# Optimization experiments

Measured on AMD Instinct MI355X. Metric: run time of the kernel, lower is better.

## Reference

```python
import jax, jax.numpy as jnp
import numpy as np

B, S, D = 4, 2048, 1024
H = 4 * D          # expert hidden dim
E_SPEC = 4         # num specific experts
E_SHR = 2          # num shared experts
TOP_K = 2


def setup_inputs() -> dict:
    key = jax.random.key(0)
    ks = jax.random.split(key, 16)
    s = 0.02
    return {
        "x": jax.random.normal(ks[0], (B, S, D), jnp.float32),
        # specific experts (stacked over expert axis)
        "spec_w1": jax.random.normal(ks[1], (E_SPEC, D, H), jnp.float32) * s,
        "spec_b1": jnp.zeros((E_SPEC, H), jnp.float32),
        "spec_w2": jax.random.normal(ks[2], (E_SPEC, H, D), jnp.float32) * s,
        "spec_b2": jnp.zeros((E_SPEC, D), jnp.float32),
        "spec_rw": jax.random.normal(ks[3], (D, E_SPEC), jnp.float32) * s,
        "spec_rb": jnp.zeros((E_SPEC,), jnp.float32),
        # shared experts
        "shr_w1": jax.random.normal(ks[4], (E_SHR, D, H), jnp.float32) * s,
        "shr_b1": jnp.zeros((E_SHR, H), jnp.float32),
        "shr_w2": jax.random.normal(ks[5], (E_SHR, H, D), jnp.float32) * s,
        "shr_b2": jnp.zeros((E_SHR, D), jnp.float32),
        "shr_rw": jax.random.normal(ks[6], (D, E_SHR), jnp.float32) * s,
        "shr_rb": jnp.zeros((E_SHR,), jnp.float32),
    }


def _expert_mlp(xf, w1, b1, w2, b2):
    # xf: [T, D]; w1: [E, D, H]; w2: [E, H, D] -> [E, T, D]
    h = jax.nn.gelu(jnp.einsum("td,edh->eth", xf, w1) + b1[:, None, :],
                    approximate=False)
    return jnp.einsum("eth,ehd->etd", h, w2) + b2[:, None, :]


def reference(x, spec_w1, spec_b1, spec_w2, spec_b2, spec_rw, spec_rb,
              shr_w1, shr_b1, shr_w2, shr_b2, shr_rw, shr_rb):
    b, s, d = x.shape
    xf = x.reshape(-1, d)                      # [T, D]
    T = xf.shape[0]

    # --- specific (top-k) routing ---
    spec_probs = jax.nn.softmax(xf @ spec_rw + spec_rb, axis=-1)   # [T, E]
    topk_probs, topk_idx = jax.lax.top_k(spec_probs, TOP_K)        # [T, K]

    # aux load-balancing loss
    counts = jnp.zeros((E_SPEC,), jnp.float32).at[topk_idx.reshape(-1)].add(1.0)
    fraction = counts / (T * TOP_K)
    aux_loss = E_SPEC * jnp.sum(fraction * spec_probs.mean(axis=0))

    # gate[t, e] = sum_k topk_probs[t,k] * 1[topk_idx[t,k]==e]
    gate = jnp.sum(jax.nn.one_hot(topk_idx, E_SPEC, dtype=xf.dtype)
                   * topk_probs[..., None], axis=1)                # [T, E]

    spec_out_e = _expert_mlp(xf, spec_w1, spec_b1, spec_w2, spec_b2)  # [E, T, D]
    specific_out = jnp.einsum("te,etd->td", gate, spec_out_e)

    # --- shared (dense) experts ---
    shr_probs = jax.nn.softmax(xf @ shr_rw + shr_rb, axis=-1)      # [T, E_shr]
    shr_out_e = _expert_mlp(xf, shr_w1, shr_b1, shr_w2, shr_b2)    # [E_shr, T, D]
    shared_out = jnp.einsum("te,etd->td", shr_probs, shr_out_e)

    final = (specific_out + shared_out).reshape(b, s, d)
    return final, aux_loss
```

## Files before the change

kernel.cpp:

```cpp
#include <hip/hip_runtime.h>
#include <hip/hip_bf16.h>

#define T_TOK 8192
#define DDIM 1024
#define HDIM 4096

typedef __bf16 bf16;
typedef bf16 bf16x8 __attribute__((ext_vector_type(8)));
typedef float f32x4 __attribute__((ext_vector_type(4)));

#define ASM_VMCNT(n) asm volatile("s_waitcnt vmcnt(" #n ")" ::: "memory")
#define MFMA16(a, b, c) __builtin_amdgcn_mfma_f32_16x16x32_bf16((a), (b), (c), 0, 0, 0)
#define G8_BAR __builtin_amdgcn_s_barrier()
#define G8_WAIT                                            \
  asm volatile("s_waitcnt lgkmcnt(0)" ::: "memory");       \
  __builtin_amdgcn_sched_barrier(0)

__device__ __forceinline__ void gl_lds16(const void* g, void* l) {
  __builtin_amdgcn_global_load_lds(
      (const __attribute__((address_space(1))) unsigned int*)g,
      (__attribute__((address_space(3))) unsigned int*)l, 16, 0, 0);
}

__device__ __forceinline__ float gelu_f(float v) {
  const float x = v * 0.7071067811865475f;
  const float ax = fabsf(x);
  const float t = 1.0f / fmaf(0.3275911f, ax, 1.0f);
  float p = fmaf(1.061405429f, t, -1.453152027f);
  p = fmaf(p, t, 1.421413741f);
  p = fmaf(p, t, -0.284496736f);
  p = fmaf(p, t, 0.254829592f);
  p = p * t;
  const float e = __expf(-ax * ax);
  const float er = fmaf(-p, e, 1.0f);
  const float erfx = (x >= 0.0f) ? er : -er;
  return 0.5f * v * (1.0f + erfx);
}

__global__ __launch_bounds__(256) void conv_router(
    const float* __restrict__ x, bf16* __restrict__ xb,
    const float* __restrict__ srw, const float* __restrict__ srb,
    const float* __restrict__ hrw, const float* __restrict__ hrb,
    float* __restrict__ gate, float4* __restrict__ probs4,
    int* __restrict__ top2) {
  const int lane = threadIdx.x & 63;
  const int w = threadIdx.x >> 6;
  const int t = blockIdx.x * 4 + w;

  const float* xr = x + (size_t)t * DDIM;
  bf16* xbr = xb + (size_t)t * DDIM;
  float p0 = 0, p1 = 0, p2 = 0, p3 = 0, p4 = 0, p5 = 0;
#pragma unroll
  for (int c = 0; c < 4; ++c) {
    const int d = c * 256 + lane * 4;
    const float4 xv = *(const float4*)(xr + d);
    bf16 ov[4] = {(bf16)xv.x, (bf16)xv.y, (bf16)xv.z, (bf16)xv.w};
    *(float2*)(xbr + d) = *(float2*)ov;
    const float xa[4] = {xv.x, xv.y, xv.z, xv.w};
#pragma unroll
    for (int j = 0; j < 4; ++j) {
      const float xd = xa[j];
      const float4 r4 = *(const float4*)(srw + (size_t)(d + j) * 4);
      p0 += xd * r4.x; p1 += xd * r4.y; p2 += xd * r4.z; p3 += xd * r4.w;
      const float2 r2 = *(const float2*)(hrw + (size_t)(d + j) * 2);
      p4 += xd * r2.x; p5 += xd * r2.y;
    }
  }
#pragma unroll
  for (int off = 32; off >= 1; off >>= 1) {
    p0 += __shfl_xor(p0, off);
    p1 += __shfl_xor(p1, off);
    p2 += __shfl_xor(p2, off);
    p3 += __shfl_xor(p3, off);
    p4 += __shfl_xor(p4, off);
    p5 += __shfl_xor(p5, off);
  }
  if (lane == 0) {
    const float l0 = p0 + srb[0], l1 = p1 + srb[1];
    const float l2 = p2 + srb[2], l3 = p3 + srb[3];
    const float m = fmaxf(fmaxf(l0, l1), fmaxf(l2, l3));
    const float e0 = expf(l0 - m), e1 = expf(l1 - m);
    const float e2 = expf(l2 - m), e3 = expf(l3 - m);
    const float s = e0 + e1 + e2 + e3;
    float pr[4] = {e0 / s, e1 / s, e2 / s, e3 / s};
    int i1 = 0; float v1 = pr[0];
#pragma unroll
    for (int e = 1; e < 4; ++e) if (pr[e] > v1) { v1 = pr[e]; i1 = e; }
    int i2 = -1; float v2 = -1.0f;
#pragma unroll
    for (int e = 0; e < 4; ++e)
      if (e != i1 && pr[e] > v2) { v2 = pr[e]; i2 = e; }
    float g[4] = {0, 0, 0, 0};
    g[i1] = v1; g[i2] = v2;
    float* gr = gate + (size_t)t * 8;
    gr[0] = g[0]; gr[1] = g[1]; gr[2] = g[2]; gr[3] = g[3];
    const float h0 = p4 + hrb[0], h1 = p5 + hrb[1];
    const float mh = fmaxf(h0, h1);
    const float q0 = expf(h0 - mh), q1 = expf(h1 - mh);
    const float qs = q0 + q1;
    gr[4] = q0 / qs; gr[5] = q1 / qs; gr[6] = 0; gr[7] = 0;
    probs4[t] = make_float4(pr[0], pr[1], pr[2], pr[3]);
    top2[t] = i1 | (i2 << 8);
  }
}

__global__ __launch_bounds__(256) void transpose_convert6(
    const float* __restrict__ spec_w, const float* __restrict__ shr_w,
    bf16* __restrict__ dst, int R, int C) {
  __shared__ float tile[32][33];
  const int z = blockIdx.z;
  const float* src = (z < 4) ? spec_w + (size_t)z * R * C
                             : shr_w + (size_t)(z - 4) * R * C;
  bf16* d = dst + (size_t)z * R * C;
  const int c0 = blockIdx.x * 32, r0 = blockIdx.y * 32;
  const int tx = threadIdx.x & 31, ty = threadIdx.x >> 5;
#pragma unroll
  for (int i = 0; i < 4; ++i)
    tile[ty + 8 * i][tx] = src[(size_t)(r0 + ty + 8 * i) * C + c0 + tx];
  __syncthreads();
#pragma unroll
  for (int i = 0; i < 4; ++i)
    d[(size_t)(c0 + ty + 8 * i) * R + r0 + tx] = (bf16)tile[tx][ty + 8 * i];
}

__global__ __launch_bounds__(1024) void scan_build(
    const int* __restrict__ top2, const float4* __restrict__ probs4,
    int* __restrict__ meta, int* __restrict__ lists, int2* __restrict__ tpos,
    float* __restrict__ auxg) {
  __shared__ unsigned long long sc[1024];
  __shared__ float4 rp[512];
  const int tid = threadIdx.x;

  int ee[8];
  unsigned long long c = 0;
  float4 ps = make_float4(0.f, 0.f, 0.f, 0.f);
#pragma unroll
  for (int j = 0; j < 8; ++j) {
    const int t = tid * 8 + j;
    const int p = top2[t];
    ee[j] = p;
    const int a = p & 15, b = (p >> 8) & 15;
    c += (1ULL << (16 * a)) + (1ULL << (16 * b));
    const float4 pv = probs4[t];
    ps.x += pv.x; ps.y += pv.y; ps.z += pv.z; ps.w += pv.w;
  }
  sc[tid] = c;
  __syncthreads();
  for (int off = 1; off < 1024; off <<= 1) {
    const unsigned long long mine = sc[tid];
    const unsigned long long prev = (tid >= off) ? sc[tid - off] : 0ULL;
    __syncthreads();
    sc[tid] = mine + prev;
    __syncthreads();
  }
  const unsigned long long incl = sc[tid];
  const unsigned long long tot = sc[1023];
  const unsigned long long excl = incl - c;
  int q0 = (int)(excl & 0xffff), q1 = (int)((excl >> 16) & 0xffff);
  int q2 = (int)((excl >> 32) & 0xffff), q3 = (int)((excl >> 48) & 0xffff);
#pragma unroll
  for (int j = 0; j < 8; ++j) {
    const int t = tid * 8 + j;
    const int a = ee[j] & 15, b = (ee[j] >> 8) & 15;
    const int pa = (a == 0) ? q0 : (a == 1) ? q1 : (a == 2) ? q2 : q3;
    lists[a * 8192 + pa] = t;
    q0 += (a == 0); q1 += (a == 1); q2 += (a == 2); q3 += (a == 3);
    const int pb = (b == 0) ? q0 : (b == 1) ? q1 : (b == 2) ? q2 : q3;
    lists[b * 8192 + pb] = t;
    q0 += (b == 0); q1 += (b == 1); q2 += (b == 2); q3 += (b == 3);
    tpos[t] = make_int2(a * 8192 + pa, b * 8192 + pb);
  }
  if (tid == 1023) {
    const int c0 = (int)(tot & 0xffff), c1 = (int)((tot >> 16) & 0xffff);
    const int c2 = (int)((tot >> 32) & 0xffff), c3 = (int)((tot >> 48) & 0xffff);
    meta[24] = c0; meta[25] = c1; meta[26] = c2; meta[27] = c3;
    auxg[0] = (float)c0; auxg[1] = (float)c1;
    auxg[2] = (float)c2; auxg[3] = (float)c3;
    const int nb0 = (c0 + 255) >> 8, nb1 = (c1 + 255) >> 8;
    const int nb2 = (c2 + 255) >> 8, nb3 = (c3 + 255) >> 8;
    const int ch0 = (nb0 + 3) >> 2, ch1 = (nb1 + 3) >> 2;
    const int ch2 = (nb2 + 3) >> 2, ch3 = (nb3 + 3) >> 2;
    meta[34] = 0;
    meta[35] = nb0 * 256;
    meta[36] = meta[35] + nb1 * 256;
    meta[37] = meta[36] + nb2 * 256;
    meta[40] = 0;
    meta[41] = 64 * ch0;
    meta[42] = meta[41] + 64 * ch1;
    meta[43] = meta[42] + 64 * ch2;
    meta[44] = meta[43] + 64 * ch3;
    meta[46] = 0;
    meta[47] = 32 * ch0;
    meta[48] = meta[47] + 32 * ch1;
    meta[49] = meta[48] + 32 * ch2;
    meta[50] = meta[49] + 32 * ch3;
  }
  if (tid >= 512) rp[tid - 512] = ps;
  __syncthreads();
  if (tid < 512) {
    const float4 o = rp[tid];
    ps.x += o.x; ps.y += o.y; ps.z += o.z; ps.w += o.w;
  }
  for (int w = 256; w >= 1; w >>= 1) {
    __syncthreads();
    if (tid >= w && tid < 2 * w) rp[tid - w] = ps;
    __syncthreads();
    if (tid < w) {
      const float4 o = rp[tid];
      ps.x += o.x; ps.y += o.y; ps.z += o.z; ps.w += o.w;
    }
  }
  if (tid == 0) {
    auxg[4] = ps.x; auxg[5] = ps.y; auxg[6] = ps.z; auxg[7] = ps.w;
  }
}

__global__ void aux_finalize(const float* __restrict__ auxg,
                             float* __restrict__ outp) {
  float a = 0.0f;
#pragma unroll
  for (int e = 0; e < 4; ++e)
    a += (auxg[e] / (float)(T_TOK * 2)) * (auxg[4 + e] / (float)T_TOK);
  outp[0] = 4.0f * a;
}

template <int KIND>
__global__ __launch_bounds__(512, 2) void g8(
    const bf16* __restrict__ A, const bf16* __restrict__ Bw,
    const float* __restrict__ bias, bf16* __restrict__ h_all, int N,
    int CH_M, int CH_N, const int* __restrict__ meta,
    const int* __restrict__ lists) {
  __shared__ __align__(1024) bf16 Alds[2 * 256 * 64];
  __shared__ __align__(1024) bf16 Blds[2 * 256 * 64];

  const int tid = threadIdx.x;
  const int lane = tid & 63, wid = tid >> 6;
  const int wm = wid >> 2, wn = wid & 3;
  const int lr = lane & 15, lg = lane >> 4;

  int bm, bn, hb = 0, s = 0;
  const bf16* Bp = Bw;
  const float* biasp = bias;
  if constexpr (KIND == 0) {
    const int xcd = blockIdx.x & 7, idx = blockIdx.x >> 3;
    bm = (xcd >> 1) * CH_M + idx / CH_N;
    bn = (xcd & 1) * CH_N + idx % CH_N;
  } else {
    const int b = blockIdx.x;
    if (b >= meta[44]) return;
    s = (b >= meta[41]) + (b >= meta[42]) + (b >= meta[43]);
    const int local = b - meta[40 + s];
    const int nbm = (meta[24 + s] + 255) >> 8;
    const int CHm = (nbm + 3) >> 2;
    if (local >= 64 * CHm) return;
    const int xc = local & 7, idx = local >> 3;
    bm = (xc >> 1) * CHm + idx / 8;
    bn = (xc & 1) * 8 + idx % 8;
    if (bm >= nbm) return;
    hb = meta[34 + s];
    Bp = Bw + (size_t)s * DDIM * HDIM;
    biasp = bias + (size_t)s * HDIM;
  }
  const int K = DDIM;
  const int NT = K >> 6;

  const int rl = tid >> 3;
  const int cbs = ((tid * 16) & 127) ^ ((rl & 7) << 4);
  int ar[4];
#pragma unroll
  for (int c = 0; c < 4; ++c) ar[c] = bm * 256 + c * 64 + rl;
  if constexpr (KIND != 0) {
    const int* lp = lists + s * 8192;
#pragma unroll
    for (int c = 0; c < 4; ++c) {
      const int t = lp[ar[c]];
      ar[c] = t < 0 ? 0 : t;
    }
  }
  const bf16* sA[4];
  const bf16* sB[4];
#pragma unroll
  for (int c = 0; c < 4; ++c) {
    sA[c] = A + (size_t)ar[c] * K + (cbs >> 1);
    sB[c] = Bp + (size_t)(bn * 256 + c * 64 + rl) * K + (cbs >> 1);
  }
  char* const ldsA = (char*)Alds;
  char* const ldsB = (char*)Blds;
  const int wb = wid * 1024;

  const int ax0 = (lg * 16) ^ ((lr & 7) << 4);
  const int ax1 = ax0 ^ 64;
  const int aro = (wm * 128 + lr) * 128;
  const int bro = (wn * 64 + lr) * 128;
  const char* const A0 = (const char*)Alds + aro + ax0;
  const char* const A1 = (const char*)Alds + aro + ax1;
  const char* const B0 = (const char*)Blds + bro + ax0;
  const char* const B1 = (const char*)Blds + bro + ax1;

  f32x4 acc[8][4] = {};
  bf16x8 af[4][2], b01[2][2], b23[2][2];

#define G8_RA(BOFF, MB)                                               \
  _Pragma("unroll") for (int i = 0; i < 4; ++i) {                     \
    af[i][0] = *(const bf16x8*)(A0 + (BOFF) + ((MB) + i) * 2048);     \
    af[i][1] = *(const bf16x8*)(A1 + (BOFF) + ((MB) + i) * 2048);     \
  }
#define G8_RB(BOFF, DST, NB)                                          \
  _Pragma("unroll") for (int i = 0; i < 2; ++i) {                     \
    DST[i][0] = *(const bf16x8*)(B0 + (BOFF) + ((NB) + i) * 2048);    \
    DST[i][1] = *(const bf16x8*)(B1 + (BOFF) + ((NB) + i) * 2048);    \
  }
#define G8_MMA(MB, NB, BSRC)                                          \
  __builtin_amdgcn_s_setprio(1);                                      \
  _Pragma("unroll") for (int i = 0; i < 4; ++i)                       \
    _Pragma("unroll") for (int j = 0; j < 2; ++j) {                   \
      acc[(MB) + i][(NB) + j] =                                       \
          MFMA16(af[i][0], BSRC[j][0], acc[(MB) + i][(NB) + j]);      \
      acc[(MB) + i][(NB) + j] =                                       \
          MFMA16(af[i][1], BSRC[j][1], acc[(MB) + i][(NB) + j]);      \
    }                                                                 \
  __builtin_amdgcn_s_setprio(0);
#define G8_STG_B(T, C, BUFO)                                          \
  gl_lds16(sB[C] + (size_t)(T) * 64, ldsB + (BUFO) + (C) * 8192 + wb);
#define G8_STG_A(T, C, BUFO)                                          \
  gl_lds16(sA[C] + (size_t)(T) * 64, ldsA + (BUFO) + (C) * 8192 + wb);

  G8_STG_B(0, 0, 0) G8_STG_B(0, 1, 0) G8_STG_B(0, 2, 0) G8_STG_B(0, 3, 0)
  G8_STG_A(0, 0, 0) G8_STG_A(0, 1, 0) G8_STG_A(0, 2, 0) G8_STG_A(0, 3, 0)
  G8_STG_B(1, 0, 32768) G8_STG_B(1, 1, 32768)
  G8_STG_B(1, 2, 32768) G8_STG_B(1, 3, 32768)
  G8_STG_A(1, 0, 32768) G8_STG_A(1, 1, 32768)
  G8_STG_A(1, 2, 32768) G8_STG_A(1, 3, 32768)
  ASM_VMCNT(8);
  G8_BAR;

  for (int t = 0; t < NT; t += 2) {
    const bool stg = (t + 2) < NT;
    G8_RA(0, 0);
    G8_RB(0, b01, 0);
    G8_BAR; G8_WAIT;
    G8_MMA(0, 0, b01);
    G8_BAR;
    G8_RB(0, b23, 2);
    G8_BAR; G8_WAIT;
    G8_MMA(0, 2, b23);
    G8_BAR;
    G8_RA(0, 4);
    if (stg) { G8_STG_B(t + 2, 0, 0) G8_STG_B(t + 2, 1, 0) }
    G8_BAR; G8_WAIT;
    G8_MMA(4, 0, b01);
    G8_BAR;
    if (stg) { G8_STG_B(t + 2, 2, 0) G8_STG_B(t + 2, 3, 0) }
    G8_MMA(4, 2, b23);
    if (stg) ASM_VMCNT(4); else ASM_VMCNT(0);
    G8_BAR;
    G8_RA(32768, 0);
    G8_RB(32768, b01, 0);
    if (stg) { G8_STG_A(t + 2, 0, 0) G8_STG_A(t + 2, 1, 0) }
    G8_BAR; G8_WAIT;
    G8_MMA(0, 0, b01);
    G8_BAR;
    G8_RB(32768, b23, 2);
    if (stg) { G8_STG_A(t + 2, 2, 0) G8_STG_A(t + 2, 3, 0) }
    G8_BAR; G8_WAIT;
    G8_MMA(0, 2, b23);
    G8_BAR;
    G8_RA(32768, 4);
    if (stg) {
      G8_STG_B(t + 3, 0, 32768) G8_STG_B(t + 3, 1, 32768)
      G8_STG_B(t + 3, 2, 32768) G8_STG_B(t + 3, 3, 32768)
    }
    G8_BAR; G8_WAIT;
    G8_MMA(4, 0, b01);
    G8_BAR;
    if (stg) {
      G8_STG_A(t + 3, 0, 32768) G8_STG_A(t + 3, 1, 32768)
      G8_STG_A(t + 3, 2, 32768) G8_STG_A(t + 3, 3, 32768)
    }
    G8_MMA(4, 2, b23);
    if (stg) ASM_VMCNT(8);
    G8_BAR;
  }

  const int colb = bn * 256 + wn * 64;
  const int rowb = hb + bm * 256 + wm * 128 + lg * 4;
  float bv[4];
#pragma unroll
  for (int nf = 0; nf < 4; ++nf) bv[nf] = biasp[colb + nf * 16 + lr];
#pragma unroll
  for (int mf = 0; mf < 8; ++mf)
#pragma unroll
    for (int nf = 0; nf < 4; ++nf) {
      const int col = colb + nf * 16 + lr;
#pragma unroll
      for (int r = 0; r < 4; ++r) {
        const int row = rowb + mf * 16 + r;
        h_all[(size_t)row * N + col] = (bf16)gelu_f(acc[mf][nf][r] + bv[nf]);
      }
    }
}

template <int EMODE>
__global__ __launch_bounds__(512, 2) void g2k(
    const bf16* __restrict__ A, int lda, const bf16* __restrict__ B,
    const float* __restrict__ bias, float* __restrict__ out,
    const float* __restrict__ gate, int gidx) {
  __shared__ __align__(1024) bf16 Alds[2 * 256 * 64];
  __shared__ __align__(1024) bf16 Blds[2 * 128 * 64];

  const int tid = threadIdx.x;
  const int lane = tid & 63, wid = tid >> 6;
  const int wm = wid >> 2, wn = wid & 3;
  const int lr = lane & 15, lg = lane >> 4;

  const int xcd = blockIdx.x & 7, idx = blockIdx.x >> 3;
  const int bm = (xcd >> 1) * 8 + idx / 4;
  const int bn = (xcd & 1) * 4 + idx % 4;
  const int K = HDIM, N = DDIM;
  const int NT = K >> 6;

  const int L = tid * 16;
  const int rl = L >> 7;
  const int colb = (L & 127) ^ ((rl & 7) << 4);

  const int ar0 = bm * 256 + rl;
  const bf16* sAc0 = A + (size_t)ar0 * lda + (colb >> 1);
  const bf16* sAc1 = A + (size_t)(ar0 + 64) * lda + (colb >> 1);
  const bf16* sAc2 = A + (size_t)(ar0 + 128) * lda + (colb >> 1);
  const bf16* sAc3 = A + (size_t)(ar0 + 192) * lda + (colb >> 1);
  const bf16* sB = B + (size_t)(bn * 128 + rl) * K + (colb >> 1);

  char* const ldsA = (char*)Alds;
  char* const ldsB = (char*)Blds;
  const int wb = wid * 1024;
  char* const stA[2] = {ldsA + wb, ldsA + 32768 + wb};
  char* const stB[2] = {ldsB + wb, ldsB + 16384 + wb};

  const int ax0 = (lg * 16) ^ ((lr & 7) << 4);
  const int ax1 = ax0 ^ 64;
  const int aro = (wm * 128 + lr) * 128;
  const int bro = (wn * 32 + lr) * 128;
  const char* const Ak0[2] = {ldsA + aro + ax0, ldsA + 32768 + aro + ax0};
  const char* const Ak1[2] = {ldsA + aro + ax1, ldsA + 32768 + aro + ax1};
  const char* const Bk0[2] = {ldsB + bro + ax0, ldsB + 16384 + bro + ax0};
  const char* const Bk1[2] = {ldsB + bro + ax1, ldsB + 16384 + bro + ax1};

  f32x4 acc[8][2] = {};

  gl_lds16(sAc0, stA[0]);
  gl_lds16(sAc1, stA[0] + 8192);
  gl_lds16(sAc2, stA[0] + 16384);
  gl_lds16(sAc3, stA[0] + 24576);
  gl_lds16(sB, stB[0]);
  gl_lds16(sB + (size_t)64 * K, stB[0] + 8192);
  gl_lds16(sB + 64, stB[1]);
  gl_lds16(sB + (size_t)64 * K + 64, stB[1] + 8192);
  gl_lds16(sAc0 + 64, stA[1]);
  gl_lds16(sAc1 + 64, stA[1] + 8192);
  ASM_VMCNT(4);
  __builtin_amdgcn_s_barrier();

  for (int kt0 = 0; kt0 < NT; kt0 += 2) {
#pragma unroll
    for (int par = 0; par < 2; ++par) {
      const int kt = kt0 + par;
      const int cur = par, oth = par ^ 1;
      const bool st1 = (kt + 1) < NT, st2 = (kt + 2) < NT;
      const size_t ko1 = (size_t)(kt + 1) << 6, ko2 = (size_t)(kt + 2) << 6;
      const char* Ac0 = Ak0[cur]; const char* Ac1 = Ak1[cur];
      const char* Bc0 = Bk0[cur]; const char* Bc1 = Bk1[cur];

      bf16x8 af[4][2], bfr[2][2];

#pragma unroll
      for (int mf = 0; mf < 4; ++mf) {
        af[mf][0] = *(const bf16x8*)(Ac0 + mf * 2048);
        af[mf][1] = *(const bf16x8*)(Ac1 + mf * 2048);
      }
      bfr[0][0] = *(const bf16x8*)(Bc0);
      bfr[0][1] = *(const bf16x8*)(Bc1);
      if (st1) {
        gl_lds16(sAc2 + ko1, stA[oth] + 16384);
        gl_lds16(sAc3 + ko1, stA[oth] + 24576);
      }
      __builtin_amdgcn_s_barrier();
      asm volatile("s_waitcnt lgkmcnt(0)" ::: "memory");
      __builtin_amdgcn_sched_barrier(0);
      __builtin_amdgcn_s_setprio(1);
#pragma unroll
      for (int mf = 0; mf < 4; ++mf) {
        acc[mf][0] = MFMA16(af[mf][0], bfr[0][0], acc[mf][0]);
        acc[mf][0] = MFMA16(af[mf][1], bfr[0][1], acc[mf][0]);
      }
      __builtin_amdgcn_s_setprio(0);
      __builtin_amdgcn_s_barrier();

      bfr[1][0] = *(const bf16x8*)(Bc0 + 2048);
      bfr[1][1] = *(const bf16x8*)(Bc1 + 2048);
      __builtin_amdgcn_s_barrier();
      asm volatile("s_waitcnt lgkmcnt(0)" ::: "memory");
      __builtin_amdgcn_sched_barrier(0);
      __builtin_amdgcn_s_setprio(1);
#pragma unroll
      for (int mf = 0; mf < 4; ++mf) {
        acc[mf][1] = MFMA16(af[mf][0], bfr[1][0], acc[mf][1]);
        acc[mf][1] = MFMA16(af[mf][1], bfr[1][1], acc[mf][1]);
      }
      __builtin_amdgcn_s_setprio(0);
      __builtin_amdgcn_s_barrier();

#pragma unroll
      for (int mf = 0; mf < 4; ++mf) {
        af[mf][0] = *(const bf16x8*)(Ac0 + 8192 + mf * 2048);
        af[mf][1] = *(const bf16x8*)(Ac1 + 8192 + mf * 2048);
      }
      if (st2) {
        gl_lds16(sB + ko2, stB[cur]);
        gl_lds16(sB + (size_t)64 * K + ko2, stB[cur] + 8192);
      }
      __builtin_amdgcn_s_barrier();
      asm volatile("s_waitcnt lgkmcnt(0)" ::: "memory");
      __builtin_amdgcn_sched_barrier(0);
      __builtin_amdgcn_s_setprio(1);
#pragma unroll
      for (int mf = 0; mf < 4; ++mf) {
        acc[4 + mf][0] = MFMA16(af[mf][0], bfr[0][0], acc[4 + mf][0]);
        acc[4 + mf][0] = MFMA16(af[mf][1], bfr[0][1], acc[4 + mf][0]);
      }
      __builtin_amdgcn_s_setprio(0);
      __builtin_amdgcn_s_barrier();

      if (st2) {
        gl_lds16(sAc0 + ko2, stA[cur]);
        gl_lds16(sAc1 + ko2, stA[cur] + 8192);
      }
      __builtin_amdgcn_s_setprio(1);
#pragma unroll
      for (int mf = 0; mf < 4; ++mf) {
        acc[4 + mf][1] = MFMA16(af[mf][0], bfr[1][0], acc[4 + mf][1]);
        acc[4 + mf][1] = MFMA16(af[mf][1], bfr[1][1], acc[4 + mf][1]);
      }
      __builtin_amdgcn_s_setprio(0);
      if (st2) {
        ASM_VMCNT(4);
        __builtin_amdgcn_s_barrier();
      } else if (st1) {
        ASM_VMCNT(0);
        __builtin_amdgcn_s_barrier();
      }
    }
  }

  const int colb2 = bn * 128 + wn * 32;
  const int rowb = bm * 256 + wm * 128 + lg * 4;
  float bv[2];
#pragma unroll
  for (int nf = 0; nf < 2; ++nf) bv[nf] = bias[colb2 + nf * 16 + lr];
#pragma unroll
  for (int mf = 0; mf < 8; ++mf) {
    float gv[4];
#pragma unroll
    for (int r = 0; r < 4; ++r)
      gv[r] = gate[(size_t)(rowb + mf * 16 + r) * 8 + gidx];
#pragma unroll
    for (int nf = 0; nf < 2; ++nf) {
      const int col = colb2 + nf * 16 + lr;
#pragma unroll
      for (int r = 0; r < 4; ++r) {
        const float v = acc[mf][nf][r] + bv[nf];
        const size_t oi = (size_t)(rowb + mf * 16 + r) * N + col;
        if constexpr (EMODE == 1)
          out[oi] += gv[r] * v;
        else
          out[oi] = gv[r] * v;
      }
    }
  }
}

__global__ __launch_bounds__(512, 2) void g2sp(
    const bf16* __restrict__ h_all, const bf16* __restrict__ w2t,
    const float* __restrict__ spec_b2, bf16* __restrict__ P,
    const float* __restrict__ gate, const int* __restrict__ meta,
    const int* __restrict__ lists) {
  __shared__ __align__(1024) bf16 Alds[2 * 256 * 64];
  __shared__ __align__(1024) bf16 Blds[2 * 128 * 64];

  const int tid = threadIdx.x;
  const int lane = tid & 63, wid = tid >> 6;
  const int wm = wid >> 2, wn = wid & 3;
  const int lr = lane & 15, lg = lane >> 4;

  const int b = blockIdx.x;
  if (b >= meta[50]) return;
  const int s = (b >= meta[47]) + (b >= meta[48]) + (b >= meta[49]);
  const int local = b - meta[46 + s];
  const int nbm = (meta[24 + s] + 255) >> 8;
  const int CHm = (nbm + 3) >> 2;
  if (local >= 32 * CHm) return;
  const int xc = local & 7, idx = local >> 3;
  int bm = (xc >> 1) * CHm + idx / 4;
  int bn = (xc & 1) * 4 + idx % 4;
  if (bm >= nbm) return;

  const int hb = meta[34 + s];
  const bf16* B = w2t + (size_t)s * DDIM * HDIM;
  const float* bias = spec_b2 + (size_t)s * DDIM;
  const int K = HDIM, N = DDIM;
  const int NT = K >> 6;

  const int L = tid * 16;
  const int rl = L >> 7;
  const int colb = (L & 127) ^ ((rl & 7) << 4);

  const int ar0 = hb + bm * 256 + rl;
  const bf16* sAc0 = h_all + (size_t)ar0 * K + (colb >> 1);
  const bf16* sAc1 = h_all + (size_t)(ar0 + 64) * K + (colb >> 1);
  const bf16* sAc2 = h_all + (size_t)(ar0 + 128) * K + (colb >> 1);
  const bf16* sAc3 = h_all + (size_t)(ar0 + 192) * K + (colb >> 1);
  const bf16* sB = B + (size_t)(bn * 128 + rl) * K + (colb >> 1);

  char* const ldsA = (char*)Alds;
  char* const ldsB = (char*)Blds;
  const int wb = wid * 1024;
  char* const stA[2] = {ldsA + wb, ldsA + 32768 + wb};
  char* const stB[2] = {ldsB + wb, ldsB + 16384 + wb};

  const int ax0 = (lg * 16) ^ ((lr & 7) << 4);
  const int ax1 = ax0 ^ 64;
  const int aro = (wm * 128 + lr) * 128;
  const int bro = (wn * 32 + lr) * 128;
  const char* const Ak0[2] = {ldsA + aro + ax0, ldsA + 32768 + aro + ax0};
  const char* const Ak1[2] = {ldsA + aro + ax1, ldsA + 32768 + aro + ax1};
  const char* const Bk0[2] = {ldsB + bro + ax0, ldsB + 16384 + bro + ax0};
  const char* const Bk1[2] = {ldsB + bro + ax1, ldsB + 16384 + bro + ax1};

  f32x4 acc[8][2] = {};

  gl_lds16(sAc0, stA[0]);
  gl_lds16(sAc1, stA[0] + 8192);
  gl_lds16(sAc2, stA[0] + 16384);
  gl_lds16(sAc3, stA[0] + 24576);
  gl_lds16(sB, stB[0]);
  gl_lds16(sB + (size_t)64 * K, stB[0] + 8192);
  gl_lds16(sB + 64, stB[1]);
  gl_lds16(sB + (size_t)64 * K + 64, stB[1] + 8192);
  gl_lds16(sAc0 + 64, stA[1]);
  gl_lds16(sAc1 + 64, stA[1] + 8192);
  ASM_VMCNT(4);
  __builtin_amdgcn_s_barrier();

  for (int kt0 = 0; kt0 < NT; kt0 += 2) {
#pragma unroll
    for (int par = 0; par < 2; ++par) {
      const int kt = kt0 + par;
      const int cur = par, oth = par ^ 1;
      const bool st1 = (kt + 1) < NT, st2 = (kt + 2) < NT;
      const size_t ko1 = (size_t)(kt + 1) << 6, ko2 = (size_t)(kt + 2) << 6;
      const char* Ac0 = Ak0[cur]; const char* Ac1 = Ak1[cur];
      const char* Bc0 = Bk0[cur]; const char* Bc1 = Bk1[cur];

      bf16x8 af[4][2], bfr[2][2];

#pragma unroll
      for (int mf = 0; mf < 4; ++mf) {
        af[mf][0] = *(const bf16x8*)(Ac0 + mf * 2048);
        af[mf][1] = *(const bf16x8*)(Ac1 + mf * 2048);
      }
      bfr[0][0] = *(const bf16x8*)(Bc0);
      bfr[0][1] = *(const bf16x8*)(Bc1);
      if (st1) {
        gl_lds16(sAc2 + ko1, stA[oth] + 16384);
        gl_lds16(sAc3 + ko1, stA[oth] + 24576);
      }
      __builtin_amdgcn_s_barrier();
      asm volatile("s_waitcnt lgkmcnt(0)" ::: "memory");
      __builtin_amdgcn_sched_barrier(0);
      __builtin_amdgcn_s_setprio(1);
#pragma unroll
      for (int mf = 0; mf < 4; ++mf) {
        acc[mf][0] = MFMA16(af[mf][0], bfr[0][0], acc[mf][0]);
        acc[mf][0] = MFMA16(af[mf][1], bfr[0][1], acc[mf][0]);
      }
      __builtin_amdgcn_s_setprio(0);
      __builtin_amdgcn_s_barrier();

      bfr[1][0] = *(const bf16x8*)(Bc0 + 2048);
      bfr[1][1] = *(const bf16x8*)(Bc1 + 2048);
      __builtin_amdgcn_s_barrier();
      asm volatile("s_waitcnt lgkmcnt(0)" ::: "memory");
      __builtin_amdgcn_sched_barrier(0);
      __builtin_amdgcn_s_setprio(1);
#pragma unroll
      for (int mf = 0; mf < 4; ++mf) {
        acc[mf][1] = MFMA16(af[mf][0], bfr[1][0], acc[mf][1]);
        acc[mf][1] = MFMA16(af[mf][1], bfr[1][1], acc[mf][1]);
      }
      __builtin_amdgcn_s_setprio(0);
      __builtin_amdgcn_s_barrier();

#pragma unroll
      for (int mf = 0; mf < 4; ++mf) {
        af[mf][0] = *(const bf16x8*)(Ac0 + 8192 + mf * 2048);
        af[mf][1] = *(const bf16x8*)(Ac1 + 8192 + mf * 2048);
      }
      if (st2) {
        gl_lds16(sB + ko2, stB[cur]);
        gl_lds16(sB + (size_t)64 * K + ko2, stB[cur] + 8192);
      }
      __builtin_amdgcn_s_barrier();
      asm volatile("s_waitcnt lgkmcnt(0)" ::: "memory");
      __builtin_amdgcn_sched_barrier(0);
      __builtin_amdgcn_s_setprio(1);
#pragma unroll
      for (int mf = 0; mf < 4; ++mf) {
        acc[4 + mf][0] = MFMA16(af[mf][0], bfr[0][0], acc[4 + mf][0]);
        acc[4 + mf][0] = MFMA16(af[mf][1], bfr[0][1], acc[4 + mf][0]);
      }
      __builtin_amdgcn_s_setprio(0);
      __builtin_amdgcn_s_barrier();

      if (st2) {
        gl_lds16(sAc0 + ko2, stA[cur]);
        gl_lds16(sAc1 + ko2, stA[cur] + 8192);
      }
      __builtin_amdgcn_s_setprio(1);
#pragma unroll
      for (int mf = 0; mf < 4; ++mf) {
        acc[4 + mf][1] = MFMA16(af[mf][0], bfr[1][0], acc[4 + mf][1]);
        acc[4 + mf][1] = MFMA16(af[mf][1], bfr[1][1], acc[4 + mf][1]);
      }
      __builtin_amdgcn_s_setprio(0);
      if (st2) {
        ASM_VMCNT(4);
        __builtin_amdgcn_s_barrier();
      } else if (st1) {
        ASM_VMCNT(0);
        __builtin_amdgcn_s_barrier();
      }
    }
  }

  const int colb2 = bn * 128 + wn * 32;
  const int rowb = bm * 256 + wm * 128 + lg * 4;
  float bv[2];
#pragma unroll
  for (int nf = 0; nf < 2; ++nf) bv[nf] = bias[colb2 + nf * 16 + lr];
  const int* lp = lists + s * 8192;
#pragma unroll
  for (int mf = 0; mf < 8; ++mf) {
    int tok[4]; float gv[4];
#pragma unroll
    for (int r = 0; r < 4; ++r) {
      tok[r] = lp[rowb + mf * 16 + r];
      gv[r] = tok[r] >= 0 ? gate[(size_t)tok[r] * 8 + s] : 0.0f;
    }
#pragma unroll
    for (int nf = 0; nf < 2; ++nf) {
      const int col = colb2 + nf * 16 + lr;
#pragma unroll
      for (int r = 0; r < 4; ++r) {
        const float v = gv[r] * (acc[mf][nf][r] + bv[nf]);
        P[(size_t)(hb + rowb + mf * 16 + r) * N + col] = (bf16)v;
      }
    }
  }
}

__global__ __launch_bounds__(256) void reduce_spec(
    const bf16* __restrict__ P, const int2* __restrict__ tpos,
    const int* __restrict__ meta, float* __restrict__ out) {
  const int t = blockIdx.x;
  const int c = threadIdx.x * 4;
  const int2 tp = tpos[t];
  const int ea = tp.x >> 13, pa = tp.x & 8191;
  const int eb = tp.y >> 13, pb = tp.y & 8191;
  const bf16* A4 = &P[(size_t)(meta[34 + ea] + pa) * DDIM + c];
  const bf16* B4 = &P[(size_t)(meta[34 + eb] + pb) * DDIM + c];
  float4 o = *(float4*)&out[(size_t)t * DDIM + c];
  o.x += (float)A4[0] + (float)B4[0];
  o.y += (float)A4[1] + (float)B4[1];
  o.z += (float)A4[2] + (float)B4[2];
  o.w += (float)A4[3] + (float)B4[3];
  *(float4*)&out[(size_t)t * DDIM + c] = o;
}

extern "C" void kernel_launch(void* const* d_in, const int* in_sizes, int n_in,
                              void* d_out, int out_size, void* d_ws,
                              size_t ws_size, hipStream_t stream) {
  const float* x = (const float*)d_in[0];
  const float* spec_w1 = (const float*)d_in[1];
  const float* spec_b1 = (const float*)d_in[2];
  const float* spec_w2 = (const float*)d_in[3];
  const float* spec_b2 = (const float*)d_in[4];
  const float* spec_rw = (const float*)d_in[5];
  const float* spec_rb = (const float*)d_in[6];
  const float* shr_w1 = (const float*)d_in[7];
  const float* shr_b1 = (const float*)d_in[8];
  const float* shr_w2 = (const float*)d_in[9];
  const float* shr_b2 = (const float*)d_in[10];
  const float* shr_rw = (const float*)d_in[11];
  const float* shr_rb = (const float*)d_in[12];
  float* out = (float*)d_out;

  char* ws = (char*)d_ws;
  const size_t DH = (size_t)DDIM * HDIM;
  const size_t OFF_W1 = 16777216;
  const size_t OFF_W2 = OFF_W1 + 50331648;
  const size_t OFF_GATE = OFF_W2 + 50331648;
  const size_t OFF_AUX = OFF_GATE + 262144;
  const size_t OFF_META = OFF_AUX + 256;
  const size_t OFF_LIST = OFF_META + 256;
  const size_t OFF_T2 = OFF_LIST + 131072;
  const size_t OFF_P4 = OFF_T2 + 32768;
  const size_t OFF_TPOS = OFF_P4 + 131072 + 1024;
  const size_t OFF_H = OFF_TPOS + 65536;
  bf16* xb = (bf16*)ws;
  bf16* w1t = (bf16*)(ws + OFF_W1);
  bf16* w2t = (bf16*)(ws + OFF_W2);
  float* gate = (float*)(ws + OFF_GATE);
  float* auxg = (float*)(ws + OFF_AUX);
  int* meta = (int*)(ws + OFF_META);
  int* lists = (int*)(ws + OFF_LIST);
  int* top2 = (int*)(ws + OFF_T2);
  float4* probs4 = (float4*)(ws + OFF_P4);
  int2* tpos = (int2*)(ws + OFF_TPOS);
  bf16* h = (bf16*)(ws + OFF_H);
  bf16* P = w1t;

  hipMemsetAsync(lists, 0xFF, 4 * 8192 * 4, stream);

  conv_router<<<T_TOK / 4, 256, 0, stream>>>(x, xb, spec_rw, spec_rb, shr_rw,
                                             shr_rb, gate, probs4, top2);
  scan_build<<<1, 1024, 0, stream>>>(top2, probs4, meta, lists, tpos, auxg);

  transpose_convert6<<<dim3(HDIM / 32, DDIM / 32, 6), 256, 0, stream>>>(
      spec_w1, shr_w1, w1t, DDIM, HDIM);
  transpose_convert6<<<dim3(DDIM / 32, HDIM / 32, 6), 256, 0, stream>>>(
      spec_w2, shr_w2, w2t, HDIM, DDIM);

  g8<0><<<1024, 512, 0, stream>>>(xb, w1t + 4 * DH, shr_b1, h, 8192,
                                  8, 16, meta, lists);
  g2k<0><<<256, 512, 0, stream>>>(h, 8192, w2t + 4 * DH, shr_b2, out,
                                  gate, 4);
  g2k<1><<<256, 512, 0, stream>>>(h + 4096, 8192, w2t + 5 * DH,
                                  shr_b2 + 1024, out, gate, 5);
  g8<1><<<2048, 512, 0, stream>>>(xb, w1t, spec_b1, h, 4096,
                                  0, 8, meta, lists);
  g2sp<<<1024, 512, 0, stream>>>(h, w2t, spec_b2, P, gate, meta, lists);
  reduce_spec<<<T_TOK, 256, 0, stream>>>(P, tpos, meta, out);

  aux_finalize<<<1, 1, 0, stream>>>(auxg, out + (size_t)T_TOK * DDIM);
}
```

Baseline: 888.7 us.

## Swap tile shapes between first and second expert GEMMs

The first-layer GEMMs (shared and routed) now use a 256x128 tile kernel with a 2-stage pipeline, launching more blocks. The routed second-layer GEMM now uses the larger 256x256 tile kernel (K=4096) with gated output written in its epilogue. Block-offset metadata is recomputed for the new grid sizes. The aim is better wave balance on the short-K first layer and more reuse on the long-K second layer, at the cost of different LDS and register pressure per kernel.

```diff
diff --git a/kernel.cpp b/kernel.cpp
--- a/kernel.cpp
+++ b/kernel.cpp
@@ -185,15 +185,15 @@
     meta[36] = meta[35] + nb1 * 256;
     meta[37] = meta[36] + nb2 * 256;
     meta[40] = 0;
-    meta[41] = 64 * ch0;
-    meta[42] = meta[41] + 64 * ch1;
-    meta[43] = meta[42] + 64 * ch2;
-    meta[44] = meta[43] + 64 * ch3;
-    meta[46] = 0;
-    meta[47] = 32 * ch0;
-    meta[48] = meta[47] + 32 * ch1;
-    meta[49] = meta[48] + 32 * ch2;
-    meta[50] = meta[49] + 32 * ch3;
+    meta[41] = 128 * ch0;
+    meta[42] = meta[41] + 128 * ch1;
+    meta[43] = meta[42] + 128 * ch2;
+    meta[44] = meta[43] + 128 * ch3;
+    meta[52] = 0;
+    meta[53] = 16 * ch0;
+    meta[54] = meta[53] + 16 * ch1;
+    meta[55] = meta[54] + 16 * ch2;
+    meta[56] = meta[55] + 16 * ch3;
   }
   if (tid >= 512) rp[tid - 512] = ps;
   __syncthreads();
@@ -225,13 +225,12 @@
 }
 
 template <int KIND>
-__global__ __launch_bounds__(512, 2) void g8(
+__global__ __launch_bounds__(512, 2) void g1p(
     const bf16* __restrict__ A, const bf16* __restrict__ Bw,
     const float* __restrict__ bias, bf16* __restrict__ h_all, int N,
-    int CH_M, int CH_N, const int* __restrict__ meta,
-    const int* __restrict__ lists) {
+    const int* __restrict__ meta, const int* __restrict__ lists) {
   __shared__ __align__(1024) bf16 Alds[2 * 256 * 64];
-  __shared__ __align__(1024) bf16 Blds[2 * 256 * 64];
+  __shared__ __align__(1024) bf16 Blds[2 * 128 * 64];
 
   const int tid = threadIdx.x;
   const int lane = tid & 63, wid = tid >> 6;
@@ -243,8 +242,8 @@
   const float* biasp = bias;
   if constexpr (KIND == 0) {
     const int xcd = blockIdx.x & 7, idx = blockIdx.x >> 3;
-    bm = (xcd >> 1) * CH_M + idx / CH_N;
-    bn = (xcd & 1) * CH_N + idx % CH_N;
+    bm = (xcd >> 1) * 8 + idx / 32;
+    bn = (xcd & 1) * 32 + idx % 32;
   } else {
     const int b = blockIdx.x;
     if (b >= meta[44]) return;
@@ -252,31 +251,214 @@
     const int local = b - meta[40 + s];
     const int nbm = (meta[24 + s] + 255) >> 8;
     const int CHm = (nbm + 3) >> 2;
-    if (local >= 64 * CHm) return;
+    if (local >= 128 * CHm) return;
     const int xc = local & 7, idx = local >> 3;
-    bm = (xc >> 1) * CHm + idx / 8;
-    bn = (xc & 1) * 8 + idx % 8;
+    bm = (xc >> 1) * CHm + idx / 16;
+    bn = (xc & 1) * 16 + idx % 16;
     if (bm >= nbm) return;
     hb = meta[34 + s];
     Bp = Bw + (size_t)s * DDIM * HDIM;
     biasp = bias + (size_t)s * HDIM;
   }
   const int K = DDIM;
-  const int NT = K >> 6;
+  const int NT = 16;
+
+  const int L = tid * 16;
+  const int rl = L >> 7;
+  const int colb = (L & 127) ^ ((rl & 7) << 4);
+
+  int ar[4];
+#pragma unroll
+  for (int c = 0; c < 4; ++c) ar[c] = bm * 256 + c * 64 + rl;
+  if constexpr (KIND == 1) {
+    const int* lp = lists + s * 8192;
+#pragma unroll
+    for (int c = 0; c < 4; ++c) {
+      const int t = lp[ar[c]];
+      ar[c] = t < 0 ? 0 : t;
+    }
+  }
+  const bf16* sAc0 = A + (size_t)ar[0] * K + (colb >> 1);
+  const bf16* sAc1 = A + (size_t)ar[1] * K + (colb >> 1);
+  const bf16* sAc2 = A + (size_t)ar[2] * K + (colb >> 1);
+  const bf16* sAc3 = A + (size_t)ar[3] * K + (colb >> 1);
+  const bf16* sB = Bp + (size_t)(bn * 128 + rl) * K + (colb >> 1);
+
+  char* const ldsA = (char*)Alds;
+  char* const ldsB = (char*)Blds;
+  const int wb = wid * 1024;
+  char* const stA[2] = {ldsA + wb, ldsA + 32768 + wb};
+  char* const stB[2] = {ldsB + wb, ldsB + 16384 + wb};
+
+  const int ax0 = (lg * 16) ^ ((lr & 7) << 4);
+  const int ax1 = ax0 ^ 64;
+  const int aro = (wm * 128 + lr) * 128;
+  const int bro = (wn * 32 + lr) * 128;
+  const char* const Ak0[2] = {ldsA + aro + ax0, ldsA + 32768 + aro + ax0};
+  const char* const Ak1[2] = {ldsA + aro + ax1, ldsA + 32768 + aro + ax1};
+  const char* const Bk0[2] = {ldsB + bro + ax0, ldsB + 16384 + bro + ax0};
+  const char* const Bk1[2] = {ldsB + bro + ax1, ldsB + 16384 + bro + ax1};
+
+  f32x4 acc[8][2] = {};
+
+  gl_lds16(sAc0, stA[0]);
+  gl_lds16(sAc1, stA[0] + 8192);
+  gl_lds16(sAc2, stA[0] + 16384);
+  gl_lds16(sAc3, stA[0] + 24576);
+  gl_lds16(sB, stB[0]);
+  gl_lds16(sB + (size_t)64 * K, stB[0] + 8192);
+  gl_lds16(sB + 64, stB[1]);
+  gl_lds16(sB + (size_t)64 * K + 64, stB[1] + 8192);
+  gl_lds16(sAc0 + 64, stA[1]);
+  gl_lds16(sAc1 + 64, stA[1] + 8192);
+  ASM_VMCNT(4);
+  __builtin_amdgcn_s_barrier();
+
+  for (int kt0 = 0; kt0 < NT; kt0 += 2) {
+#pragma unroll
+    for (int par = 0; par < 2; ++par) {
+      const int kt = kt0 + par;
+      const int cur = par, oth = par ^ 1;
+      const bool st1 = (kt + 1) < NT, st2 = (kt + 2) < NT;
+      const size_t ko1 = (size_t)(kt + 1) << 6, ko2 = (size_t)(kt + 2) << 6;
+      const char* Ac0 = Ak0[cur]; const char* Ac1 = Ak1[cur];
+      const char* Bc0 = Bk0[cur]; const char* Bc1 = Bk1[cur];
+
+      bf16x8 af[4][2], bfr[2][2];
+
+#pragma unroll
+      for (int mf = 0; mf < 4; ++mf) {
+        af[mf][0] = *(const bf16x8*)(Ac0 + mf * 2048);
+        af[mf][1] = *(const bf16x8*)(Ac1 + mf * 2048);
+      }
+      bfr[0][0] = *(const bf16x8*)(Bc0);
+      bfr[0][1] = *(const bf16x8*)(Bc1);
+      if (st1) {
+        gl_lds16(sAc2 + ko1, stA[oth] + 16384);
+        gl_lds16(sAc3 + ko1, stA[oth] + 24576);
+      }
+      __builtin_amdgcn_s_barrier();
+      asm volatile("s_waitcnt lgkmcnt(0)" ::: "memory");
+      __builtin_amdgcn_sched_barrier(0);
+      __builtin_amdgcn_s_setprio(1);
+#pragma unroll
+      for (int mf = 0; mf < 4; ++mf) {
+        acc[mf][0] = MFMA16(af[mf][0], bfr[0][0], acc[mf][0]);
+        acc[mf][0] = MFMA16(af[mf][1], bfr[0][1], acc[mf][0]);
+      }
+      __builtin_amdgcn_s_setprio(0);
+      __builtin_amdgcn_s_barrier();
+
+      bfr[1][0] = *(const bf16x8*)(Bc0 + 2048);
+      bfr[1][1] = *(const bf16x8*)(Bc1 + 2048);
+      __builtin_amdgcn_s_barrier();
+      asm volatile("s_waitcnt lgkmcnt(0)" ::: "memory");
+      __builtin_amdgcn_sched_barrier(0);
+      __builtin_amdgcn_s_setprio(1);
+#pragma unroll
+      for (int mf = 0; mf < 4; ++mf) {
+        acc[mf][1] = MFMA16(af[mf][0], bfr[1][0], acc[mf][1]);
+        acc[mf][1] = MFMA16(af[mf][1], bfr[1][1], acc[mf][1]);
+      }
+      __builtin_amdgcn_s_setprio(0);
+      __builtin_amdgcn_s_barrier();
+
+#pragma unroll
+      for (int mf = 0; mf < 4; ++mf) {
+        af[mf][0] = *(const bf16x8*)(Ac0 + 8192 + mf * 2048);
+        af[mf][1] = *(const bf16x8*)(Ac1 + 8192 + mf * 2048);
+      }
+      if (st2) {
+        gl_lds16(sB + ko2, stB[cur]);
+        gl_lds16(sB + (size_t)64 * K + ko2, stB[cur] + 8192);
+      }
+      __builtin_amdgcn_s_barrier();
+      asm volatile("s_waitcnt lgkmcnt(0)" ::: "memory");
+      __builtin_amdgcn_sched_barrier(0);
+      __builtin_amdgcn_s_setprio(1);
+#pragma unroll
+      for (int mf = 0; mf < 4; ++mf) {
+        acc[4 + mf][0] = MFMA16(af[mf][0], bfr[0][0], acc[4 + mf][0]);
+        acc[4 + mf][0] = MFMA16(af[mf][1], bfr[0][1], acc[4 + mf][0]);
+      }
+      __builtin_amdgcn_s_setprio(0);
+      __builtin_amdgcn_s_barrier();
+
+      if (st2) {
+        gl_lds16(sAc0 + ko2, stA[cur]);
+        gl_lds16(sAc1 + ko2, stA[cur] + 8192);
+      }
+      __builtin_amdgcn_s_setprio(1);
+#pragma unroll
+      for (int mf = 0; mf < 4; ++mf) {
+        acc[4 + mf][1] = MFMA16(af[mf][0], bfr[1][0], acc[4 + mf][1]);
+        acc[4 + mf][1] = MFMA16(af[mf][1], bfr[1][1], acc[4 + mf][1]);
+      }
+      __builtin_amdgcn_s_setprio(0);
+      if (st2) {
+        ASM_VMCNT(4);
+        __builtin_amdgcn_s_barrier();
+      } else if (st1) {
+        ASM_VMCNT(0);
+        __builtin_amdgcn_s_barrier();
+      }
+    }
+  }
+
+  const int colb2 = bn * 128 + wn * 32;
+  const int rowb = bm * 256 + wm * 128 + lg * 4;
+  float bv[2];
+#pragma unroll
+  for (int nf = 0; nf < 2; ++nf) bv[nf] = biasp[colb2 + nf * 16 + lr];
+#pragma unroll
+  for (int mf = 0; mf < 8; ++mf)
+#pragma unroll
+    for (int nf = 0; nf < 2; ++nf) {
+      const int col = colb2 + nf * 16 + lr;
+#pragma unroll
+      for (int r = 0; r < 4; ++r) {
+        const int row = hb + rowb + mf * 16 + r;
+        h_all[(size_t)row * N + col] = (bf16)gelu_f(acc[mf][nf][r] + bv[nf]);
+      }
+    }
+}
+
+template <int KIND>
+__global__ __launch_bounds__(512, 2) void g8(
+    const bf16* __restrict__ A, const bf16* __restrict__ Bw,
+    const float* __restrict__ bias, bf16* __restrict__ Out, int N,
+    int CH_M, int CH_N, const int* __restrict__ meta,
+    const int* __restrict__ lists, const float* __restrict__ gate) {
+  __shared__ __align__(1024) bf16 Alds[2 * 256 * 64];
+  __shared__ __align__(1024) bf16 Blds[2 * 256 * 64];
+
+  const int tid = threadIdx.x;
+  const int lane = tid & 63, wid = tid >> 6;
+  const int wm = wid >> 2, wn = wid & 3;
+  const int lr = lane & 15, lg = lane >> 4;
+
+  const int b = blockIdx.x;
+  if (b >= meta[56]) return;
+  const int s = (b >= meta[53]) + (b >= meta[54]) + (b >= meta[55]);
+  const int local = b - meta[52 + s];
+  const int nbm = (meta[24 + s] + 255) >> 8;
+  const int CHm = (nbm + 3) >> 2;
+  if (local >= 16 * CHm) return;
+  const int xc = local & 7, idx = local >> 3;
+  const int bm = (xc >> 1) * CHm + idx / 2;
+  const int bn = (xc & 1) * 2 + idx % 2;
+  if (bm >= nbm) return;
+  const int hb = meta[34 + s];
+  const bf16* Bp = Bw + (size_t)s * DDIM * HDIM;
+  const float* biasp = bias + (size_t)s * DDIM;
+  constexpr int K = HDIM;
+  constexpr int NT = K >> 6;
 
   const int rl = tid >> 3;
   const int cbs = ((tid * 16) & 127) ^ ((rl & 7) << 4);
   int ar[4];
 #pragma unroll
-  for (int c = 0; c < 4; ++c) ar[c] = bm * 256 + c * 64 + rl;
-  if constexpr (KIND != 0) {
-    const int* lp = lists + s * 8192;
-#pragma unroll
-    for (int c = 0; c < 4; ++c) {
-      const int t = lp[ar[c]];
-      ar[c] = t < 0 ? 0 : t;
-    }
-  }
+  for (int c = 0; c < 4; ++c) ar[c] = hb + bm * 256 + c * 64 + rl;
   const bf16* sA[4];
   const bf16* sB[4];
 #pragma unroll
@@ -383,21 +565,29 @@
   }
 
   const int colb = bn * 256 + wn * 64;
-  const int rowb = hb + bm * 256 + wm * 128 + lg * 4;
+  const int lrowb = bm * 256 + wm * 128 + lg * 4;
   float bv[4];
 #pragma unroll
   for (int nf = 0; nf < 4; ++nf) bv[nf] = biasp[colb + nf * 16 + lr];
-#pragma unroll
-  for (int mf = 0; mf < 8; ++mf)
+  const int* lp = lists + s * 8192;
+#pragma unroll
+  for (int mf = 0; mf < 8; ++mf) {
+    int tok[4]; float gv[4];
+#pragma unroll
+    for (int r = 0; r < 4; ++r) {
+      tok[r] = lp[lrowb + mf * 16 + r];
+      gv[r] = tok[r] >= 0 ? gate[(size_t)tok[r] * 8 + s] : 0.0f;
+    }
 #pragma unroll
     for (int nf = 0; nf < 4; ++nf) {
       const int col = colb + nf * 16 + lr;
 #pragma unroll
       for (int r = 0; r < 4; ++r) {
-        const int row = rowb + mf * 16 + r;
-        h_all[(size_t)row * N + col] = (bf16)gelu_f(acc[mf][nf][r] + bv[nf]);
-      }
-    }
+        const float v = gv[r] * (acc[mf][nf][r] + bv[nf]);
+        Out[(size_t)(hb + lrowb + mf * 16 + r) * N + col] = (bf16)v;
+      }
+    }
+  }
 }
 
 template <int EMODE>
@@ -573,195 +763,6 @@
           out[oi] += gv[r] * v;
         else
           out[oi] = gv[r] * v;
-      }
-    }
-  }
-}
-
-__global__ __launch_bounds__(512, 2) void g2sp(
-    const bf16* __restrict__ h_all, const bf16* __restrict__ w2t,
-    const float* __restrict__ spec_b2, bf16* __restrict__ P,
-    const float* __restrict__ gate, const int* __restrict__ meta,
-    const int* __restrict__ lists) {
-  __shared__ __align__(1024) bf16 Alds[2 * 256 * 64];
-  __shared__ __align__(1024) bf16 Blds[2 * 128 * 64];
-
-  const int tid = threadIdx.x;
-  const int lane = tid & 63, wid = tid >> 6;
-  const int wm = wid >> 2, wn = wid & 3;
-  const int lr = lane & 15, lg = lane >> 4;
-
-  const int b = blockIdx.x;
-  if (b >= meta[50]) return;
-  const int s = (b >= meta[47]) + (b >= meta[48]) + (b >= meta[49]);
-  const int local = b - meta[46 + s];
-  const int nbm = (meta[24 + s] + 255) >> 8;
-  const int CHm = (nbm + 3) >> 2;
-  if (local >= 32 * CHm) return;
-  const int xc = local & 7, idx = local >> 3;
-  int bm = (xc >> 1) * CHm + idx / 4;
-  int bn = (xc & 1) * 4 + idx % 4;
-  if (bm >= nbm) return;
-
-  const int hb = meta[34 + s];
-  const bf16* B = w2t + (size_t)s * DDIM * HDIM;
-  const float* bias = spec_b2 + (size_t)s * DDIM;
-  const int K = HDIM, N = DDIM;
-  const int NT = K >> 6;
-
-  const int L = tid * 16;
-  const int rl = L >> 7;
-  const int colb = (L & 127) ^ ((rl & 7) << 4);
-
-  const int ar0 = hb + bm * 256 + rl;
-  const bf16* sAc0 = h_all + (size_t)ar0 * K + (colb >> 1);
-  const bf16* sAc1 = h_all + (size_t)(ar0 + 64) * K + (colb >> 1);
-  const bf16* sAc2 = h_all + (size_t)(ar0 + 128) * K + (colb >> 1);
-  const bf16* sAc3 = h_all + (size_t)(ar0 + 192) * K + (colb >> 1);
-  const bf16* sB = B + (size_t)(bn * 128 + rl) * K + (colb >> 1);
-
-  char* const ldsA = (char*)Alds;
-  char* const ldsB = (char*)Blds;
-  const int wb = wid * 1024;
-  char* const stA[2] = {ldsA + wb, ldsA + 32768 + wb};
-  char* const stB[2] = {ldsB + wb, ldsB + 16384 + wb};
-
-  const int ax0 = (lg * 16) ^ ((lr & 7) << 4);
-  const int ax1 = ax0 ^ 64;
-  const int aro = (wm * 128 + lr) * 128;
-  const int bro = (wn * 32 + lr) * 128;
-  const char* const Ak0[2] = {ldsA + aro + ax0, ldsA + 32768 + aro + ax0};
-  const char* const Ak1[2] = {ldsA + aro + ax1, ldsA + 32768 + aro + ax1};
-  const char* const Bk0[2] = {ldsB + bro + ax0, ldsB + 16384 + bro + ax0};
-  const char* const Bk1[2] = {ldsB + bro + ax1, ldsB + 16384 + bro + ax1};
-
-  f32x4 acc[8][2] = {};
-
-  gl_lds16(sAc0, stA[0]);
-  gl_lds16(sAc1, stA[0] + 8192);
-  gl_lds16(sAc2, stA[0] + 16384);
-  gl_lds16(sAc3, stA[0] + 24576);
-  gl_lds16(sB, stB[0]);
-  gl_lds16(sB + (size_t)64 * K, stB[0] + 8192);
-  gl_lds16(sB + 64, stB[1]);
-  gl_lds16(sB + (size_t)64 * K + 64, stB[1] + 8192);
-  gl_lds16(sAc0 + 64, stA[1]);
-  gl_lds16(sAc1 + 64, stA[1] + 8192);
-  ASM_VMCNT(4);
-  __builtin_amdgcn_s_barrier();
-
-  for (int kt0 = 0; kt0 < NT; kt0 += 2) {
-#pragma unroll
-    for (int par = 0; par < 2; ++par) {
-      const int kt = kt0 + par;
-      const int cur = par, oth = par ^ 1;
-      const bool st1 = (kt + 1) < NT, st2 = (kt + 2) < NT;
-      const size_t ko1 = (size_t)(kt + 1) << 6, ko2 = (size_t)(kt + 2) << 6;
-      const char* Ac0 = Ak0[cur]; const char* Ac1 = Ak1[cur];
-      const char* Bc0 = Bk0[cur]; const char* Bc1 = Bk1[cur];
-
-      bf16x8 af[4][2], bfr[2][2];
-
-#pragma unroll
-      for (int mf = 0; mf < 4; ++mf) {
-        af[mf][0] = *(const bf16x8*)(Ac0 + mf * 2048);
-        af[mf][1] = *(const bf16x8*)(Ac1 + mf * 2048);
-      }
-      bfr[0][0] = *(const bf16x8*)(Bc0);
-      bfr[0][1] = *(const bf16x8*)(Bc1);
-      if (st1) {
-        gl_lds16(sAc2 + ko1, stA[oth] + 16384);
-        gl_lds16(sAc3 + ko1, stA[oth] + 24576);
-      }
-      __builtin_amdgcn_s_barrier();
-      asm volatile("s_waitcnt lgkmcnt(0)" ::: "memory");
-      __builtin_amdgcn_sched_barrier(0);
-      __builtin_amdgcn_s_setprio(1);
-#pragma unroll
-      for (int mf = 0; mf < 4; ++mf) {
-        acc[mf][0] = MFMA16(af[mf][0], bfr[0][0], acc[mf][0]);
-        acc[mf][0] = MFMA16(af[mf][1], bfr[0][1], acc[mf][0]);
-      }
-      __builtin_amdgcn_s_setprio(0);
-      __builtin_amdgcn_s_barrier();
-
-      bfr[1][0] = *(const bf16x8*)(Bc0 + 2048);
-      bfr[1][1] = *(const bf16x8*)(Bc1 + 2048);
-      __builtin_amdgcn_s_barrier();
-      asm volatile("s_waitcnt lgkmcnt(0)" ::: "memory");
-      __builtin_amdgcn_sched_barrier(0);
-      __builtin_amdgcn_s_setprio(1);
-#pragma unroll
-      for (int mf = 0; mf < 4; ++mf) {
-        acc[mf][1] = MFMA16(af[mf][0], bfr[1][0], acc[mf][1]);
-        acc[mf][1] = MFMA16(af[mf][1], bfr[1][1], acc[mf][1]);
-      }
-      __builtin_amdgcn_s_setprio(0);
-      __builtin_amdgcn_s_barrier();
-
-#pragma unroll
-      for (int mf = 0; mf < 4; ++mf) {
-        af[mf][0] = *(const bf16x8*)(Ac0 + 8192 + mf * 2048);
-        af[mf][1] = *(const bf16x8*)(Ac1 + 8192 + mf * 2048);
-      }
-      if (st2) {
-        gl_lds16(sB + ko2, stB[cur]);
-        gl_lds16(sB + (size_t)64 * K + ko2, stB[cur] + 8192);
-      }
-      __builtin_amdgcn_s_barrier();
-      asm volatile("s_waitcnt lgkmcnt(0)" ::: "memory");
-      __builtin_amdgcn_sched_barrier(0);
-      __builtin_amdgcn_s_setprio(1);
-#pragma unroll
-      for (int mf = 0; mf < 4; ++mf) {
-        acc[4 + mf][0] = MFMA16(af[mf][0], bfr[0][0], acc[4 + mf][0]);
-        acc[4 + mf][0] = MFMA16(af[mf][1], bfr[0][1], acc[4 + mf][0]);
-      }
-      __builtin_amdgcn_s_setprio(0);
-      __builtin_amdgcn_s_barrier();
-
-      if (st2) {
-        gl_lds16(sAc0 + ko2, stA[cur]);
-        gl_lds16(sAc1 + ko2, stA[cur] + 8192);
-      }
-      __builtin_amdgcn_s_setprio(1);
-#pragma unroll
-      for (int mf = 0; mf < 4; ++mf) {
-        acc[4 + mf][1] = MFMA16(af[mf][0], bfr[1][0], acc[4 + mf][1]);
-        acc[4 + mf][1] = MFMA16(af[mf][1], bfr[1][1], acc[4 + mf][1]);
-      }
-      __builtin_amdgcn_s_setprio(0);
-      if (st2) {
-        ASM_VMCNT(4);
-        __builtin_amdgcn_s_barrier();
-      } else if (st1) {
-        ASM_VMCNT(0);
-        __builtin_amdgcn_s_barrier();
-      }
-    }
-  }
-
-  const int colb2 = bn * 128 + wn * 32;
-  const int rowb = bm * 256 + wm * 128 + lg * 4;
-  float bv[2];
-#pragma unroll
-  for (int nf = 0; nf < 2; ++nf) bv[nf] = bias[colb2 + nf * 16 + lr];
-  const int* lp = lists + s * 8192;
-#pragma unroll
-  for (int mf = 0; mf < 8; ++mf) {
-    int tok[4]; float gv[4];
-#pragma unroll
-    for (int r = 0; r < 4; ++r) {
-      tok[r] = lp[rowb + mf * 16 + r];
-      gv[r] = tok[r] >= 0 ? gate[(size_t)tok[r] * 8 + s] : 0.0f;
-    }
-#pragma unroll
-    for (int nf = 0; nf < 2; ++nf) {
-      const int col = colb2 + nf * 16 + lr;
-#pragma unroll
-      for (int r = 0; r < 4; ++r) {
-        const float v = gv[r] * (acc[mf][nf][r] + bv[nf]);
-        P[(size_t)(hb + rowb + mf * 16 + r) * N + col] = (bf16)v;
       }
     }
   }
@@ -839,15 +840,16 @@
   transpose_convert6<<<dim3(DDIM / 32, HDIM / 32, 6), 256, 0, stream>>>(
       spec_w2, shr_w2, w2t, HDIM, DDIM);
 
-  g8<0><<<1024, 512, 0, stream>>>(xb, w1t + 4 * DH, shr_b1, h, 8192,
-                                  8, 16, meta, lists);
+  g1p<0><<<2048, 512, 0, stream>>>(xb, w1t + 4 * DH, shr_b1, h, 8192,
+                                   meta, lists);
   g2k<0><<<256, 512, 0, stream>>>(h, 8192, w2t + 4 * DH, shr_b2, out,
                                   gate, 4);
   g2k<1><<<256, 512, 0, stream>>>(h + 4096, 8192, w2t + 5 * DH,
                                   shr_b2 + 1024, out, gate, 5);
-  g8<1><<<2048, 512, 0, stream>>>(xb, w1t, spec_b1, h, 4096,
-                                  0, 8, meta, lists);
-  g2sp<<<1024, 512, 0, stream>>>(h, w2t, spec_b2, P, gate, meta, lists);
+  g1p<1><<<2560, 512, 0, stream>>>(xb, w1t, spec_b1, h, 4096,
+                                   meta, lists);
+  g8<2><<<512, 512, 0, stream>>>(h, w2t, spec_b2, P, DDIM,
+                                 0, 2, meta, lists, gate);
   reduce_spec<<<T_TOK, 256, 0, stream>>>(P, tpos, meta, out);
 
   aux_finalize<<<1, 1, 0, stream>>>(auxg, out + (size_t)T_TOK * DDIM);
```

Result: slower. 1.000 ms (+12.6%).
